# Optimization experiments

Measured on AMD Instinct MI355X. Metric: run time of the kernel, lower is better.

Reference implementation:

```python
import jax, jax.numpy as jnp
import numpy as np

N_PRIORS = 262144
N_CLASSES = 81  # includes background at index 0


def _decode(loc, priors, variance):
    # Standard SSD decode: priors are [N,4] (cx, cy, w, h) in relative coords.
    centers = priors[:, :2] + loc[:, :2] * variance[0] * priors[:, 2:]
    sizes = priors[:, 2:] * jnp.exp(loc[:, 2:] * variance[1])
    mins = centers - sizes * 0.5          # (xmin, ymin)
    maxs = mins + sizes                   # (xmax, ymax)
    return jnp.concatenate([mins, maxs], axis=-1)  # [N,4]


def setup_inputs() -> dict:
    key = jax.random.key(0)
    k1, k2, k3 = jax.random.split(key, 3)
    inp = jax.random.normal(k1, (1, N_PRIORS, 4 + N_CLASSES), dtype=jnp.float32)
    cxy = jax.random.uniform(k2, (N_PRIORS, 2), dtype=jnp.float32)
    wh = jax.random.uniform(k3, (N_PRIORS, 2), dtype=jnp.float32) * 0.1 + 0.05
    priors = jnp.concatenate([cxy, wh], axis=-1)
    variance = jnp.array([0.1, 0.2], dtype=jnp.float32)
    score_threshold = jnp.array([0.3], dtype=jnp.float32)
    return {"input": inp, "priors": priors, "variance": variance,
            "score_threshold": score_threshold}


def reference(input, priors, variance, score_threshold):
    # input: [1, N, 4+C]
    loc = input[0, :, :4]                                   # [N,4]
    cls = jax.nn.softmax(input[0, :, 4:], axis=-1)          # [N,C]
    class_conf = jnp.max(cls, axis=1)                       # [N]
    class_pred = jnp.argmax(cls, axis=1)                    # [N] int
    boxes = _decode(loc, priors, variance)                  # [N,4]
    # torch version compacts via nonzero/index_select; jit-compatible
    # equivalent: keep fixed length N and mask out invalid rows.
    valid = (class_pred > 0) & (class_conf > score_threshold[0])  # [N] bool
    boxes = jnp.where(valid[:, None], boxes, 0.0)
    class_conf = jnp.where(valid, class_conf, 0.0)
    class_pred_out = jnp.where(valid, class_pred - 1, -1)
    detections = jnp.concatenate(
        [boxes, class_conf[:, None], class_pred_out[:, None].astype(jnp.float32)],
        axis=-1)                                            # [N,6]
    return boxes, class_conf, class_pred_out, detections[None]
```

## Files before the change

### kernel.cpp

```cpp
#include <hip/hip_runtime.h>

#define NCLS 81
#define ROW  85
#define TPB  64
#define BLK_BYTES (TPB * ROW * 4)

typedef __attribute__((address_space(3))) void*       as3_void;
typedef const __attribute__((address_space(1))) void* as1_cvoid;

__device__ __forceinline__ float exp_cr(float xf) {
    double x = (double)xf;
    x = (x < -150.0) ? -150.0 : x;
    double t = x * 1.4426950408889634074;
    double nd = rint(t);
    double r = fma(nd, -6.93147180369123816490e-01, x);
    r = fma(nd, -1.90821492927058770002e-10, r);
    double p = 1.0 / 6227020800.0;
    p = fma(p, r, 1.0 / 479001600.0);
    p = fma(p, r, 1.0 / 39916800.0);
    p = fma(p, r, 1.0 / 3628800.0);
    p = fma(p, r, 1.0 / 362880.0);
    p = fma(p, r, 1.0 / 40320.0);
    p = fma(p, r, 1.0 / 5040.0);
    p = fma(p, r, 1.0 / 720.0);
    p = fma(p, r, 1.0 / 120.0);
    p = fma(p, r, 1.0 / 24.0);
    p = fma(p, r, 1.0 / 6.0);
    p = fma(p, r, 0.5);
    p = fma(p, r, 1.0);
    p = fma(p, r, 1.0);
    long long ni = (long long)nd;
    double sc = __longlong_as_double((1023LL + ni) << 52);
    return (float)(p * sc);
}

__global__ __launch_bounds__(TPB) void ssd_decode_kernel(
    const float* __restrict__ inp,
    const float* __restrict__ priors,
    const float* __restrict__ var,
    const float* __restrict__ thr,
    float* __restrict__ out,
    int n)
{
    __shared__ __align__(16) float lds[TPB * ROW];
    const int tid = threadIdx.x;
    const long long base = (long long)blockIdx.x * TPB;
    if (base >= n) return;

    {
        const char* gsrc = (const char*)inp + (long long)blockIdx.x * BLK_BYTES;
        char* lbase = (char*)lds;
        #pragma unroll
        for (int k = 0; k < 21; ++k) {
            __builtin_amdgcn_global_load_lds(
                (as1_cvoid)(gsrc + k * 1024 + tid * 16),
                (as3_void)(lbase + k * 1024), 16, 0, 0);
        }
        __builtin_amdgcn_global_load_lds(
            (as1_cvoid)(gsrc + 21504 + tid * 4),
            (as3_void)(lbase + 21504), 4, 0, 0);
        asm volatile("s_waitcnt vmcnt(0)" ::: "memory");
        __builtin_amdgcn_sched_barrier(0);
    }
    __syncthreads();

    float* row = lds + tid * ROW;

    float lg[ROW];
    #pragma unroll
    for (int k = 0; k < ROW; ++k) lg[k] = row[k];

    float mx[8];
    #pragma unroll
    for (int j = 0; j < 8; ++j) mx[j] = lg[4 + j];
    #pragma unroll
    for (int k = 1; k < 10; ++k)
        #pragma unroll
        for (int j = 0; j < 8; ++j) mx[j] = fmaxf(mx[j], lg[4 + k * 8 + j]);
    float m = fmaxf(fmaxf(fmaxf(mx[0], mx[1]), fmaxf(mx[2], mx[3])),
                    fmaxf(fmaxf(mx[4], mx[5]), fmaxf(mx[6], mx[7])));
    m = fmaxf(m, lg[84]);

    int nc = 0;
    int amf = 127;
    float racc[8];
    #pragma unroll
    for (int j = 0; j < 8; ++j) racc[j] = 0.0f;
    #pragma unroll
    for (int k = 0; k < 10; ++k)
        #pragma unroll
        for (int j = 0; j < 8; ++j) {
            int c = k * 8 + j;
            float d = lg[4 + c] - m;
            nc  += (d >= -9.5367431640625e-07f) ? 1 : 0;
            int cand = (d == 0.0f) ? c : 127;
            amf = (cand < amf) ? cand : amf;
            racc[j] += __expf(d);
        }
    float s1 = ((racc[0] + racc[1]) + (racc[2] + racc[3]))
             + ((racc[4] + racc[5]) + (racc[6] + racc[7]));
    {
        float d80 = lg[84] - m;
        nc  += (d80 >= -9.5367431640625e-07f) ? 1 : 0;
        int cand = (d80 == 0.0f) ? 80 : 127;
        amf = (cand < amf) ? cand : amf;
        s1 += __expf(d80);
    }

    int am;
    float conf;
    if (__any(nc > 1)) {
        float racx[8];
        #pragma unroll
        for (int j = 0; j < 8; ++j) racx[j] = 0.0f;
        #pragma unroll
        for (int k = 0; k < 10; ++k)
            #pragma unroll
            for (int j = 0; j < 8; ++j) {
                float e = exp_cr(row[4 + k * 8 + j] - m);
                row[4 + k * 8 + j] = e;
                racx[j] += e;
            }
        float s = ((racx[0] + racx[1]) + (racx[2] + racx[3]))
                + ((racx[4] + racx[5]) + (racx[6] + racx[7]));
        float e80 = exp_cr(row[84] - m);
        row[84] = e80;
        s += e80;

        float pmax = 1.0f / s;
        float t = 1.0f;
        #pragma unroll
        for (int k = 0; k < 8; ++k) {
            float tn = __uint_as_float(__float_as_uint(t) - 1u);
            t = ((tn / s) == pmax) ? tn : t;
        }
        am = 81;
        #pragma unroll
        for (int c = 80; c >= 0; --c)
            am = (row[4 + c] >= t) ? c : am;
        conf = pmax;
    } else {
        am = amf;
        conf = 1.0f / s1;
    }

    float l0 = lg[0], l1 = lg[1], l2 = lg[2], l3 = lg[3];
    float4 pr = reinterpret_cast<const float4*>(priors)[base + tid];
    float v0 = var[0], v1 = var[1];
    float cx = pr.x + l0 * v0 * pr.z;
    float cy = pr.y + l1 * v0 * pr.w;
    float w  = pr.z * __expf(l2 * v1);
    float h  = pr.w * __expf(l3 * v1);
    float x0 = cx - w * 0.5f;
    float y0 = cy - h * 0.5f;
    float x1 = x0 + w;
    float y1 = y0 + h;

    bool valid = (am > 0) && (conf > thr[0]);

    float4 box;
    box.x = valid ? x0 : 0.0f;
    box.y = valid ? y0 : 0.0f;
    box.z = valid ? x1 : 0.0f;
    box.w = valid ? y1 : 0.0f;
    float cz = valid ? conf : 0.0f;
    float pz = valid ? (float)(am - 1) : -1.0f;

    const long long i = base + tid;
    reinterpret_cast<float4*>(out)[i] = box;
    out[(long long)4 * n + i] = cz;
    out[(long long)5 * n + i] = pz;
    float2* det2 = reinterpret_cast<float2*>(out + (long long)6 * n + i * 6);
    det2[0] = make_float2(box.x, box.y);
    det2[1] = make_float2(box.z, box.w);
    det2[2] = make_float2(cz, pz);
}

extern "C" void kernel_launch(void* const* d_in, const int* in_sizes, int n_in,
                              void* d_out, int out_size, void* d_ws, size_t ws_size,
                              hipStream_t stream)
{
    const float* inp    = (const float*)d_in[0];
    const float* priors = (const float*)d_in[1];
    const float* var    = (const float*)d_in[2];
    const float* thr    = (const float*)d_in[3];
    float* out = (float*)d_out;

    int n = in_sizes[1] / 4;
    int blocks = (n + TPB - 1) / TPB;
    ssd_decode_kernel<<<blocks, TPB, 0, stream>>>(inp, priors, var, thr, out, n);
}
```

Before: 141.9 us.

## Use persistent grid with double-buffered LDS prefetch of the next chunk

The kernel now launches a fixed grid of 768 single-wave blocks that loop over 64-row chunks. While computing one chunk from LDS, each block issues async global-to-LDS loads for its next chunk into a second buffer. The aim is to hide load latency and cut per-block launch overhead. It doubles LDS per block (about 43 KB), which limits occupancy. A tail where n is not a multiple of 64 is dropped, and the __syncthreads was removed, which only works because each block is one wave. The vmcnt(0) wait also waits on the previous iteration's output stores.

After: 148.7 us. 4.8% more time.

```diff
diff --git a/kernel.cpp b/kernel.cpp
--- a/kernel.cpp
+++ b/kernel.cpp
@@ -3,7 +3,8 @@
 #define NCLS 81
 #define ROW  85
 #define TPB  64
-#define BLK_BYTES (TPB * ROW * 4)
+#define CHUNK_B (TPB * ROW * 4)
+#define GRID 768
 
 typedef __attribute__((address_space(3))) void*       as3_void;
 typedef const __attribute__((address_space(1))) void* as1_cvoid;
@@ -34,6 +35,21 @@
     return (float)(p * sc);
 }
 
+__device__ __forceinline__ void stage_chunk(const float* __restrict__ inp,
+                                            float* lbuf, int t, int tid) {
+    const char* gsrc = (const char*)inp + (long long)t * CHUNK_B;
+    char* lbase = (char*)lbuf;
+    #pragma unroll
+    for (int k = 0; k < 21; ++k) {
+        __builtin_amdgcn_global_load_lds(
+            (as1_cvoid)(gsrc + k * 1024 + tid * 16),
+            (as3_void)(lbase + k * 1024), 16, 0, 0);
+    }
+    __builtin_amdgcn_global_load_lds(
+        (as1_cvoid)(gsrc + 21504 + tid * 4),
+        (as3_void)(lbase + 21504), 4, 0, 0);
+}
+
 __global__ __launch_bounds__(TPB) void ssd_decode_kernel(
     const float* __restrict__ inp,
     const float* __restrict__ priors,
@@ -42,138 +58,137 @@
     float* __restrict__ out,
     int n)
 {
-    __shared__ __align__(16) float lds[TPB * ROW];
+    __shared__ __align__(16) float lds[2][TPB * ROW];
     const int tid = threadIdx.x;
-    const long long base = (long long)blockIdx.x * TPB;
-    if (base >= n) return;
-
-    {
-        const char* gsrc = (const char*)inp + (long long)blockIdx.x * BLK_BYTES;
-        char* lbase = (char*)lds;
-        #pragma unroll
-        for (int k = 0; k < 21; ++k) {
-            __builtin_amdgcn_global_load_lds(
-                (as1_cvoid)(gsrc + k * 1024 + tid * 16),
-                (as3_void)(lbase + k * 1024), 16, 0, 0);
-        }
-        __builtin_amdgcn_global_load_lds(
-            (as1_cvoid)(gsrc + 21504 + tid * 4),
-            (as3_void)(lbase + 21504), 4, 0, 0);
+    const int nchunks = n / TPB;
+
+    int t = blockIdx.x;
+    if (t >= nchunks) return;
+
+    int buf = 0;
+    stage_chunk(inp, &lds[0][0], t, tid);
+
+    for (; t < nchunks; t += GRID) {
         asm volatile("s_waitcnt vmcnt(0)" ::: "memory");
         __builtin_amdgcn_sched_barrier(0);
+
+        const int nxt = t + GRID;
+        if (nxt < nchunks)
+            stage_chunk(inp, &lds[buf ^ 1][0], nxt, tid);
+
+        float* row = &lds[buf][tid * ROW];
+
+        float lg[ROW];
+        #pragma unroll
+        for (int k = 0; k < ROW; ++k) lg[k] = row[k];
+
+        float mx[8];
+        #pragma unroll
+        for (int j = 0; j < 8; ++j) mx[j] = lg[4 + j];
+        #pragma unroll
+        for (int k = 1; k < 10; ++k)
+            #pragma unroll
+            for (int j = 0; j < 8; ++j) mx[j] = fmaxf(mx[j], lg[4 + k * 8 + j]);
+        float m = fmaxf(fmaxf(fmaxf(mx[0], mx[1]), fmaxf(mx[2], mx[3])),
+                        fmaxf(fmaxf(mx[4], mx[5]), fmaxf(mx[6], mx[7])));
+        m = fmaxf(m, lg[84]);
+
+        int nc = 0;
+        int amf = 127;
+        float racc[8];
+        #pragma unroll
+        for (int j = 0; j < 8; ++j) racc[j] = 0.0f;
+        #pragma unroll
+        for (int k = 0; k < 10; ++k)
+            #pragma unroll
+            for (int j = 0; j < 8; ++j) {
+                int c = k * 8 + j;
+                float d = lg[4 + c] - m;
+                nc  += (d >= -9.5367431640625e-07f) ? 1 : 0;
+                int cand = (d == 0.0f) ? c : 127;
+                amf = (cand < amf) ? cand : amf;
+                racc[j] += __expf(d);
+            }
+        float s1 = ((racc[0] + racc[1]) + (racc[2] + racc[3]))
+                 + ((racc[4] + racc[5]) + (racc[6] + racc[7]));
+        {
+            float d80 = lg[84] - m;
+            nc  += (d80 >= -9.5367431640625e-07f) ? 1 : 0;
+            int cand = (d80 == 0.0f) ? 80 : 127;
+            amf = (cand < amf) ? cand : amf;
+            s1 += __expf(d80);
+        }
+
+        int am;
+        float conf;
+        if (__any(nc > 1)) {
+            float racx[8];
+            #pragma unroll
+            for (int j = 0; j < 8; ++j) racx[j] = 0.0f;
+            #pragma unroll
+            for (int k = 0; k < 10; ++k)
+                #pragma unroll
+                for (int j = 0; j < 8; ++j) {
+                    float e = exp_cr(row[4 + k * 8 + j] - m);
+                    row[4 + k * 8 + j] = e;
+                    racx[j] += e;
+                }
+            float s = ((racx[0] + racx[1]) + (racx[2] + racx[3]))
+                    + ((racx[4] + racx[5]) + (racx[6] + racx[7]));
+            float e80 = exp_cr(row[84] - m);
+            row[84] = e80;
+            s += e80;
+
+            float pmax = 1.0f / s;
+            float tb = 1.0f;
+            #pragma unroll
+            for (int k = 0; k < 8; ++k) {
+                float tn = __uint_as_float(__float_as_uint(tb) - 1u);
+                tb = ((tn / s) == pmax) ? tn : tb;
+            }
+            am = 81;
+            #pragma unroll
+            for (int c = 80; c >= 0; --c)
+                am = (row[4 + c] >= tb) ? c : am;
+            conf = pmax;
+        } else {
+            am = amf;
+            conf = 1.0f / s1;
+        }
+
+        float l0 = lg[0], l1 = lg[1], l2 = lg[2], l3 = lg[3];
+        const long long i = (long long)t * TPB + tid;
+        float4 pr = reinterpret_cast<const float4*>(priors)[i];
+        float v0 = var[0], v1 = var[1];
+        float cx = pr.x + l0 * v0 * pr.z;
+        float cy = pr.y + l1 * v0 * pr.w;
+        float w  = pr.z * __expf(l2 * v1);
+        float h  = pr.w * __expf(l3 * v1);
+        float x0 = cx - w * 0.5f;
+        float y0 = cy - h * 0.5f;
+        float x1 = x0 + w;
+        float y1 = y0 + h;
+
+        bool valid = (am > 0) && (conf > thr[0]);
+
+        float4 box;
+        box.x = valid ? x0 : 0.0f;
+        box.y = valid ? y0 : 0.0f;
+        box.z = valid ? x1 : 0.0f;
+        box.w = valid ? y1 : 0.0f;
+        float cz = valid ? conf : 0.0f;
+        float pz = valid ? (float)(am - 1) : -1.0f;
+
+        reinterpret_cast<float4*>(out)[i] = box;
+        out[(long long)4 * n + i] = cz;
+        out[(long long)5 * n + i] = pz;
+        float2* det2 = reinterpret_cast<float2*>(out + (long long)6 * n + i * 6);
+        det2[0] = make_float2(box.x, box.y);
+        det2[1] = make_float2(box.z, box.w);
+        det2[2] = make_float2(cz, pz);
+
+        buf ^= 1;
     }
-    __syncthreads();
-
-    float* row = lds + tid * ROW;
-
-    float lg[ROW];
-    #pragma unroll
-    for (int k = 0; k < ROW; ++k) lg[k] = row[k];
-
-    float mx[8];
-    #pragma unroll
-    for (int j = 0; j < 8; ++j) mx[j] = lg[4 + j];
-    #pragma unroll
-    for (int k = 1; k < 10; ++k)
-        #pragma unroll
-        for (int j = 0; j < 8; ++j) mx[j] = fmaxf(mx[j], lg[4 + k * 8 + j]);
-    float m = fmaxf(fmaxf(fmaxf(mx[0], mx[1]), fmaxf(mx[2], mx[3])),
-                    fmaxf(fmaxf(mx[4], mx[5]), fmaxf(mx[6], mx[7])));
-    m = fmaxf(m, lg[84]);
-
-    int nc = 0;
-    int amf = 127;
-    float racc[8];
-    #pragma unroll
-    for (int j = 0; j < 8; ++j) racc[j] = 0.0f;
-    #pragma unroll
-    for (int k = 0; k < 10; ++k)
-        #pragma unroll
-        for (int j = 0; j < 8; ++j) {
-            int c = k * 8 + j;
-            float d = lg[4 + c] - m;
-            nc  += (d >= -9.5367431640625e-07f) ? 1 : 0;
-            int cand = (d == 0.0f) ? c : 127;
-            amf = (cand < amf) ? cand : amf;
-            racc[j] += __expf(d);
-        }
-    float s1 = ((racc[0] + racc[1]) + (racc[2] + racc[3]))
-             + ((racc[4] + racc[5]) + (racc[6] + racc[7]));
-    {
-        float d80 = lg[84] - m;
-        nc  += (d80 >= -9.5367431640625e-07f) ? 1 : 0;
-        int cand = (d80 == 0.0f) ? 80 : 127;
-        amf = (cand < amf) ? cand : amf;
-        s1 += __expf(d80);
-    }
-
-    int am;
-    float conf;
-    if (__any(nc > 1)) {
-        float racx[8];
-        #pragma unroll
-        for (int j = 0; j < 8; ++j) racx[j] = 0.0f;
-        #pragma unroll
-        for (int k = 0; k < 10; ++k)
-            #pragma unroll
-            for (int j = 0; j < 8; ++j) {
-                float e = exp_cr(row[4 + k * 8 + j] - m);
-                row[4 + k * 8 + j] = e;
-                racx[j] += e;
-            }
-        float s = ((racx[0] + racx[1]) + (racx[2] + racx[3]))
-                + ((racx[4] + racx[5]) + (racx[6] + racx[7]));
-        float e80 = exp_cr(row[84] - m);
-        row[84] = e80;
-        s += e80;
-
-        float pmax = 1.0f / s;
-        float t = 1.0f;
-        #pragma unroll
-        for (int k = 0; k < 8; ++k) {
-            float tn = __uint_as_float(__float_as_uint(t) - 1u);
-            t = ((tn / s) == pmax) ? tn : t;
-        }
-        am = 81;
-        #pragma unroll
-        for (int c = 80; c >= 0; --c)
-            am = (row[4 + c] >= t) ? c : am;
-        conf = pmax;
-    } else {
-        am = amf;
-        conf = 1.0f / s1;
-    }
-
-    float l0 = lg[0], l1 = lg[1], l2 = lg[2], l3 = lg[3];
-    float4 pr = reinterpret_cast<const float4*>(priors)[base + tid];
-    float v0 = var[0], v1 = var[1];
-    float cx = pr.x + l0 * v0 * pr.z;
-    float cy = pr.y + l1 * v0 * pr.w;
-    float w  = pr.z * __expf(l2 * v1);
-    float h  = pr.w * __expf(l3 * v1);
-    float x0 = cx - w * 0.5f;
-    float y0 = cy - h * 0.5f;
-    float x1 = x0 + w;
-    float y1 = y0 + h;
-
-    bool valid = (am > 0) && (conf > thr[0]);
-
-    float4 box;
-    box.x = valid ? x0 : 0.0f;
-    box.y = valid ? y0 : 0.0f;
-    box.z = valid ? x1 : 0.0f;
-    box.w = valid ? y1 : 0.0f;
-    float cz = valid ? conf : 0.0f;
-    float pz = valid ? (float)(am - 1) : -1.0f;
-
-    const long long i = base + tid;
-    reinterpret_cast<float4*>(out)[i] = box;
-    out[(long long)4 * n + i] = cz;
-    out[(long long)5 * n + i] = pz;
-    float2* det2 = reinterpret_cast<float2*>(out + (long long)6 * n + i * 6);
-    det2[0] = make_float2(box.x, box.y);
-    det2[1] = make_float2(box.z, box.w);
-    det2[2] = make_float2(cz, pz);
 }
 
 extern "C" void kernel_launch(void* const* d_in, const int* in_sizes, int n_in,
@@ -187,6 +202,5 @@
     float* out = (float*)d_out;
 
     int n = in_sizes[1] / 4;
-    int blocks = (n + TPB - 1) / TPB;
-    ssd_decode_kernel<<<blocks, TPB, 0, stream>>>(inp, priors, var, thr, out, n);
-}
+    ssd_decode_kernel<<<GRID, TPB, 0, stream>>>(inp, priors, var, thr, out, n);
+}
```
